# Kernel optimization log

Measured on AMD Instinct MI355X. Metric: run time of the kernel, lower is better.

Reference implementation:

```python
import jax, jax.numpy as jnp
import numpy as np

N, L, HOP = 512, 16, 8  # L // 2


def overlap_and_add(frames, hop):
    # frames: [..., K, L] -> [..., (K-1)*hop + L]
    K, Lf = frames.shape[-2], frames.shape[-1]
    T = (K - 1) * hop + Lf
    idx = (jnp.arange(K)[:, None] * hop + jnp.arange(Lf)[None, :]).reshape(-1)
    flat = frames.reshape(frames.shape[:-2] + (K * Lf,))
    out = jnp.zeros(frames.shape[:-2] + (T,), frames.dtype)
    return out.at[..., idx].add(flat)


def setup_inputs() -> dict:
    key = jax.random.key(0)
    k1, k2, k3 = jax.random.split(key, 3)
    M, C, K = 8, 2, 6000
    inputs = jax.random.normal(k1, (M, N, K), dtype=jnp.float32)
    est_mask = jax.random.uniform(k2, (M, C, N, K), dtype=jnp.float32)
    W = jax.random.normal(k3, (N, L), dtype=jnp.float32) * 0.05
    return {"inputs": inputs, "est_mask": est_mask, "W": W}


def reference(inputs, est_mask, W):
    # masked source spectra: [M, C, N, K]
    masked = inputs[:, None, :, :] * est_mask
    # transpose to [M, C, K, N] and project N -> L (fused in einsum)
    frames = jnp.einsum('mcnk,nl->mckl', masked, W)  # [M, C, K, L]
    # overlap-and-add with hop L // 2 -> [M, C, T]
    return overlap_and_add(frames, HOP)
```

## Files before the change

kernel.cpp:

```cpp
#include <hip/hip_runtime.h>

#define NN   512
#define LL   16
#define MM   8
#define CC   2
#define KK   6000
#define TT   ((KK - 1) * 8 + 16)
#define KW   64
#define NCH  32
#define NC   (NN / NCH)
#define ROWB (KK * 4)
#define TENS_B (NCH * KW * 4)
#define BUF_B  (3 * TENS_B)

typedef __attribute__((address_space(3))) void       lds_v;
typedef __attribute__((address_space(1))) const void glob_v;

__global__ __launch_bounds__(512, 2) void decoder_dma_kernel(
    const float* __restrict__ inputs,
    const float* __restrict__ est_mask,
    const float* __restrict__ W,
    float* __restrict__ out)
{
    __shared__ __align__(16) char lds[2 * BUF_B];

    const int tid = threadIdx.x;
    const int t   = tid & 63;
    const int wq  = __builtin_amdgcn_readfirstlane(tid >> 6);
    const int kb  = blockIdx.x;
    const int m   = blockIdx.y;

    const int lane_r = t >> 4;
    int cb = kb * 256 + (t & 15) * 16;
    if (cb > ROWB - 16) cb = ROWB - 16;
    const size_t lane_off = (size_t)lane_r * ROWB + cb;

    const char* tb0 = (const char*)inputs   + (size_t)m * NN * ROWB;
    const char* tb1 = (const char*)est_mask + (size_t)(m * CC + 0) * NN * ROWB;
    const char* tb2 = tb1 + (size_t)NN * ROWB;
    const char* tb[3] = { tb0, tb1, tb2 };

    auto issue = [&](int c, int bsel) {
        char* bb = lds + bsel * BUF_B;
        #pragma unroll
        for (int j = 0; j < 3; ++j) {
            const int idx  = wq * 3 + j;
            const int tens = idx >> 3;
            const int g    = idx & 7;
            const char* gsrc = tb[tens] + (size_t)(c * NCH + g * 4) * ROWB + lane_off;
            lds_v* ldst = (lds_v*)(bb + tens * TENS_B + g * 1024);
            __builtin_amdgcn_global_load_lds((glob_v*)gsrc, ldst, 16, 0, 0);
        }
    };

    float acc0[LL], acc1[LL];
    #pragma unroll
    for (int l = 0; l < LL; ++l) { acc0[l] = 0.f; acc1[l] = 0.f; }

    issue(0, 0);
    __syncthreads();

    for (int c = 0; c < NC; ++c) {
        if (c + 1 < NC) issue(c + 1, (c + 1) & 1);

        const float* Lin = (const float*)(lds + (c & 1) * BUF_B);
        const float* Lm0 = Lin + 2048;
        const float* Lm1 = Lin + 4096;

        #pragma unroll
        for (int rr = 0; rr < 4; ++rr) {
            const int r = wq * 4 + rr;
            const int n = c * NCH + r;
            float wv[LL];
            *reinterpret_cast<float4*>(&wv[0])  = *(const float4*)(W + n * LL + 0);
            *reinterpret_cast<float4*>(&wv[4])  = *(const float4*)(W + n * LL + 4);
            *reinterpret_cast<float4*>(&wv[8])  = *(const float4*)(W + n * LL + 8);
            *reinterpret_cast<float4*>(&wv[12]) = *(const float4*)(W + n * LL + 12);

            const float xin = Lin[r * 64 + t];
            const float xm0 = Lm0[r * 64 + t];
            const float xm1 = Lm1[r * 64 + t];
            const float x0 = xin * xm0;
            const float x1 = xin * xm1;
            #pragma unroll
            for (int l = 0; l < LL; ++l) {
                acc0[l] = fmaf(x0, wv[l], acc0[l]);
                acc1[l] = fmaf(x1, wv[l], acc1[l]);
            }
        }
        __syncthreads();
    }

    float* sm = (float*)lds;
    if (wq >= 4) {
        float* d = &sm[((wq - 4) * 64 + t) * 33];
        #pragma unroll
        for (int l = 0; l < LL; ++l) { d[l] = acc0[l]; d[16 + l] = acc1[l]; }
    }
    __syncthreads();
    if (wq < 4) {
        const float* s = &sm[(wq * 64 + t) * 33];
        #pragma unroll
        for (int l = 0; l < LL; ++l) { acc0[l] += s[l]; acc1[l] += s[16 + l]; }
    }
    __syncthreads();
    if (wq == 2 || wq == 3) {
        float* d = &sm[((wq - 2) * 64 + t) * 33];
        #pragma unroll
        for (int l = 0; l < LL; ++l) { d[l] = acc0[l]; d[16 + l] = acc1[l]; }
    }
    __syncthreads();
    if (wq < 2) {
        const float* s = &sm[(wq * 64 + t) * 33];
        #pragma unroll
        for (int l = 0; l < LL; ++l) { acc0[l] += s[l]; acc1[l] += s[16 + l]; }
    }
    __syncthreads();
    if (wq == 1) {
        float* d = &sm[t * 33];
        #pragma unroll
        for (int l = 0; l < LL; ++l) { d[l] = acc0[l]; d[16 + l] = acc1[l]; }
    }
    __syncthreads();

    if (wq == 0) {
        {
            const float* s = &sm[t * 33];
            #pragma unroll
            for (int l = 0; l < LL; ++l) { acc0[l] += s[l]; acc1[l] += s[16 + l]; }
        }

        const int k = kb * KW + t;
        float ph0[8], ph1[8];
        #pragma unroll
        for (int j = 0; j < 8; ++j) {
            ph0[j] = __shfl_up(acc0[8 + j], 1);
            ph1[j] = __shfl_up(acc1[8 + j], 1);
        }

        if (k < KK) {
            float* o0 = out + ((size_t)m * CC + 0) * TT + 8 * k;
            float* o1 = out + ((size_t)m * CC + 1) * TT + 8 * k;

            if (t == 0) {
                #pragma unroll
                for (int j = 0; j < 8; ++j) {
                    atomicAdd(&o0[j], acc0[j]);
                    atomicAdd(&o1[j], acc1[j]);
                }
            } else {
                #pragma unroll
                for (int j = 0; j < 8; ++j) {
                    o0[j] = acc0[j] + ph0[j];
                    o1[j] = acc1[j] + ph1[j];
                }
            }
            if (t == 63 || k == KK - 1) {
                #pragma unroll
                for (int j = 0; j < 8; ++j) {
                    atomicAdd(&o0[8 + j], acc0[8 + j]);
                    atomicAdd(&o1[8 + j], acc1[8 + j]);
                }
            }
        }
    }
}

extern "C" void kernel_launch(void* const* d_in, const int* in_sizes, int n_in,
                              void* d_out, int out_size, void* d_ws, size_t ws_size,
                              hipStream_t stream) {
    const float* inputs   = (const float*)d_in[0];
    const float* est_mask = (const float*)d_in[1];
    const float* W        = (const float*)d_in[2];
    float*       out      = (float*)d_out;

    hipMemsetAsync(out, 0, (size_t)out_size * sizeof(float), stream);

    dim3 grid((KK + KW - 1) / KW, MM);
    decoder_dma_kernel<<<grid, 512, 0, stream>>>(inputs, est_mask, W, out);
}
```

Before: 64.96 us.

## Make each wave load its own rows and replace block barriers with vmcnt waits

Each wave now issues the async global-to-LDS loads for exactly the four rows of each tensor it later consumes. The per-chunk __syncthreads can therefore be replaced with per-wave s_waitcnt vmcnt waits, so waves no longer stall on each other within the double-buffered pipeline. The launch-bounds occupancy hint is also raised from 2 to 6, which constrains register allocation to allow more resident waves. The risks are register spilling under the tighter bound, and the vmcnt count also covering the W global loads. The kernel already streams close to memory bandwidth, so the headroom is small.

```diff
diff --git a/kernel.cpp b/kernel.cpp
--- a/kernel.cpp
+++ b/kernel.cpp
@@ -16,7 +16,7 @@
 typedef __attribute__((address_space(3))) void       lds_v;
 typedef __attribute__((address_space(1))) const void glob_v;
 
-__global__ __launch_bounds__(512, 2) void decoder_dma_kernel(
+__global__ __launch_bounds__(512, 6) void decoder_dma_kernel(
     const float* __restrict__ inputs,
     const float* __restrict__ est_mask,
     const float* __restrict__ W,
@@ -36,21 +36,17 @@
     const size_t lane_off = (size_t)lane_r * ROWB + cb;
 
     const char* tb0 = (const char*)inputs   + (size_t)m * NN * ROWB;
-    const char* tb1 = (const char*)est_mask + (size_t)(m * CC + 0) * NN * ROWB;
+    const char* tb1 = (const char*)est_mask + (size_t)(m * CC) * NN * ROWB;
     const char* tb2 = tb1 + (size_t)NN * ROWB;
-    const char* tb[3] = { tb0, tb1, tb2 };
+
+    char* dst_base = lds + wq * 1024;
 
     auto issue = [&](int c, int bsel) {
-        char* bb = lds + bsel * BUF_B;
-        #pragma unroll
-        for (int j = 0; j < 3; ++j) {
-            const int idx  = wq * 3 + j;
-            const int tens = idx >> 3;
-            const int g    = idx & 7;
-            const char* gsrc = tb[tens] + (size_t)(c * NCH + g * 4) * ROWB + lane_off;
-            lds_v* ldst = (lds_v*)(bb + tens * TENS_B + g * 1024);
-            __builtin_amdgcn_global_load_lds((glob_v*)gsrc, ldst, 16, 0, 0);
-        }
+        const size_t rowoff = (size_t)(c * NCH + wq * 4) * ROWB + lane_off;
+        char* bb = dst_base + bsel * BUF_B;
+        __builtin_amdgcn_global_load_lds((glob_v*)(tb0 + rowoff), (lds_v*)(bb),              16, 0, 0);
+        __builtin_amdgcn_global_load_lds((glob_v*)(tb1 + rowoff), (lds_v*)(bb + TENS_B),     16, 0, 0);
+        __builtin_amdgcn_global_load_lds((glob_v*)(tb2 + rowoff), (lds_v*)(bb + 2 * TENS_B), 16, 0, 0);
     };
 
     float acc0[LL], acc1[LL];
@@ -58,28 +54,30 @@
     for (int l = 0; l < LL; ++l) { acc0[l] = 0.f; acc1[l] = 0.f; }
 
     issue(0, 0);
-    __syncthreads();
 
     for (int c = 0; c < NC; ++c) {
-        if (c + 1 < NC) issue(c + 1, (c + 1) & 1);
+        if (c + 1 < NC) {
+            issue(c + 1, (c + 1) & 1);
+            asm volatile("s_waitcnt vmcnt(3)" ::: "memory");
+        } else {
+            asm volatile("s_waitcnt vmcnt(0)" ::: "memory");
+        }
+        __builtin_amdgcn_sched_barrier(0);
 
-        const float* Lin = (const float*)(lds + (c & 1) * BUF_B);
-        const float* Lm0 = Lin + 2048;
-        const float* Lm1 = Lin + 4096;
+        const float* Lb = (const float*)(lds + (c & 1) * BUF_B + wq * 1024);
 
         #pragma unroll
         for (int rr = 0; rr < 4; ++rr) {
-            const int r = wq * 4 + rr;
-            const int n = c * NCH + r;
+            const int n = c * NCH + wq * 4 + rr;
             float wv[LL];
             *reinterpret_cast<float4*>(&wv[0])  = *(const float4*)(W + n * LL + 0);
             *reinterpret_cast<float4*>(&wv[4])  = *(const float4*)(W + n * LL + 4);
             *reinterpret_cast<float4*>(&wv[8])  = *(const float4*)(W + n * LL + 8);
             *reinterpret_cast<float4*>(&wv[12]) = *(const float4*)(W + n * LL + 12);
 
-            const float xin = Lin[r * 64 + t];
-            const float xm0 = Lm0[r * 64 + t];
-            const float xm1 = Lm1[r * 64 + t];
+            const float xin = Lb[rr * 64 + t];
+            const float xm0 = Lb[(TENS_B / 4) + rr * 64 + t];
+            const float xm1 = Lb[(2 * TENS_B / 4) + rr * 64 + t];
             const float x0 = xin * xm0;
             const float x1 = xin * xm1;
             #pragma unroll
@@ -88,8 +86,9 @@
                 acc1[l] = fmaf(x1, wv[l], acc1[l]);
             }
         }
-        __syncthreads();
     }
+
+    __syncthreads();
 
     float* sm = (float*)lds;
     if (wq >= 4) {
```

Result: no change. 65.24 us (+0.4%).
